# Kernel optimization log

Hardware: AMD Instinct MI355X
Metric: run time of the kernel (lower is better)

## Reference

```python
import jax, jax.numpy as jnp
import numpy as np

B, T, C = 16, 4096, 64  # batch, seq_len, n_embd == head_size


def setup_inputs() -> dict:
    key = jax.random.key(0)
    k1, k2, k3, k4 = jax.random.split(key, 4)
    x = jax.random.normal(k1, (B, T, C), dtype=jnp.float32)
    Wq = jax.random.normal(k2, (C, C), dtype=jnp.float32) * (C ** -0.5)
    Wk = jax.random.normal(k3, (C, C), dtype=jnp.float32) * (C ** -0.5)
    Wv = jax.random.normal(k4, (C, C), dtype=jnp.float32) * (C ** -0.5)
    return {"x": x, "Wq": Wq, "Wk": Wk, "Wv": Wv}


def reference(x, Wq, Wk, Wv):
    # Single-head causal self-attention (dropout rate = 0.0 in source -> identity).
    q = jnp.einsum('btc,cd->btd', x, Wq)  # [B,T,D]
    k = jnp.einsum('btc,cd->btd', x, Wk)  # [B,T,D]
    v = jnp.einsum('btc,cd->btd', x, Wv)  # [B,T,D]
    scale = q.shape[-1] ** -0.5
    wei = jnp.einsum('btd,bsd->bts', q, k) * scale  # [B,T,T] scores
    causal = jnp.tril(jnp.ones((T, T), dtype=bool))  # [T,T]
    wei = jnp.where(causal[None, :, :], wei, jnp.finfo(wei.dtype).min)
    wei = jax.nn.softmax(wei, axis=-1)
    out = jnp.einsum('bts,bsd->btd', wei, v)  # [B,T,D]
    return out
```

## Files before the change

### kernel.cpp

```cpp
#include <hip/hip_runtime.h>
#include <hip/hip_bf16.h>
#include <math.h>

#define BATCH 16
#define SEQ 4096
#define HDIM 64

typedef __attribute__((ext_vector_type(8))) short bf16x8;
typedef __attribute__((ext_vector_type(4))) float f32x4;
typedef __attribute__((ext_vector_type(4))) unsigned int u32x4;
typedef __attribute__((ext_vector_type(8))) unsigned short us8;

#define QSCALE 0.1803368801111601f

static __device__ __forceinline__ float exp2_fast(float x) {
#if __has_builtin(__builtin_amdgcn_exp2f)
    return __builtin_amdgcn_exp2f(x);
#else
    float r; asm("v_exp_f32 %0, %1" : "=v"(r) : "v"(x)); return r;
#endif
}

static __device__ __forceinline__ void load_lds16(const void* g, void* l) {
    __builtin_amdgcn_global_load_lds(
        (const __attribute__((address_space(1))) unsigned int*)g,
        (__attribute__((address_space(3))) unsigned int*)l,
        16, 0, 0);
}

static __device__ __forceinline__ unsigned short bf16bits(float f) {
    __hip_bfloat16 h = __float2bfloat16(f);
    return *(unsigned short*)&h;
}

static __device__ __forceinline__ unsigned int pack_bf16_trunc(float f0, float f1) {
    unsigned int u0 = __builtin_bit_cast(unsigned int, f0);
    unsigned int u1 = __builtin_bit_cast(unsigned int, f1);
#if __has_builtin(__builtin_amdgcn_perm)
    return __builtin_amdgcn_perm(u1, u0, 0x07060302u);
#else
    return (u1 & 0xFFFF0000u) | (u0 >> 16);
#endif
}

__global__ __launch_bounds__(256)
void qkv_mfma_kernel(const float* __restrict__ x,
                     const float* __restrict__ Wq,
                     const float* __restrict__ Wk,
                     const float* __restrict__ Wv,
                     __hip_bfloat16* __restrict__ qb,
                     __hip_bfloat16* __restrict__ kb,
                     __hip_bfloat16* __restrict__ vt) {
    __shared__ __attribute__((aligned(16))) __hip_bfloat16 swt[3 * 64 * 64];
    __shared__ __attribute__((aligned(16))) __hip_bfloat16 sout[64][80];
    const int tid = threadIdx.x;
    const int wv = tid >> 6;
    const int lane = tid & 63;
    const int quad = lane >> 4;
    const int ml = lane & 15;
    const size_t row0 = (size_t)blockIdx.x * 64;
    const int batch = (int)(row0 >> 12);
    const int t0 = (int)(row0 & 4095);

    #pragma unroll
    for (int mat = 0; mat < 3; ++mat) {
        const float* W = (mat == 0) ? Wq : (mat == 1) ? Wk : Wv;
        const float sc = (mat == 0) ? QSCALE : 1.0f;
        #pragma unroll
        for (int c2 = 0; c2 < 2; ++c2) {
            const int chunk = c2 * 256 + tid;
            const int n = chunk & 63;
            const int c = chunk >> 6;
            us8 u;
            #pragma unroll
            for (int j = 0; j < 8; ++j)
                u[j] = bf16bits(W[(c * 8 + j) * HDIM + n] * sc);
            *(us8*)(swt + mat * 4096 + n * 64 + (size_t)(c ^ (n & 7)) * 8) = u;
        }
    }

    bf16x8 a0, a1;
    {
        const float4* xr = (const float4*)(x + (row0 + wv * 16 + ml) * HDIM);
        float4 lo = xr[quad * 2], hi = xr[quad * 2 + 1];
        float t8[8] = {lo.x, lo.y, lo.z, lo.w, hi.x, hi.y, hi.z, hi.w};
        #pragma unroll
        for (int j = 0; j < 8; ++j) a0[j] = (short)bf16bits(t8[j]);
        lo = xr[8 + quad * 2]; hi = xr[9 + quad * 2];
        float u8[8] = {lo.x, lo.y, lo.z, lo.w, hi.x, hi.y, hi.z, hi.w};
        #pragma unroll
        for (int j = 0; j < 8; ++j) a1[j] = (short)bf16bits(u8[j]);
    }
    __syncthreads();

    #pragma unroll
    for (int mat = 0; mat < 3; ++mat) {
        const __hip_bfloat16* wb = swt + mat * 4096;
        f32x4 acc[4];
        #pragma unroll
        for (int nt = 0; nt < 4; ++nt) {
            const int n = nt * 16 + ml;
            const int nx = n & 7;
            const bf16x8 bl = *(const bf16x8*)(wb + (size_t)n * 64 + (size_t)((quad) ^ nx) * 8);
            const bf16x8 bh = *(const bf16x8*)(wb + (size_t)n * 64 + (size_t)((quad + 4) ^ nx) * 8);
            acc[nt] = __builtin_amdgcn_mfma_f32_16x16x32_bf16(a0, bl, (f32x4){0.f,0.f,0.f,0.f}, 0, 0, 0);
            acc[nt] = __builtin_amdgcn_mfma_f32_16x16x32_bf16(a1, bh, acc[nt], 0, 0, 0);
        }

        if (mat < 2) {
            #pragma unroll
            for (int nt = 0; nt < 4; ++nt)
                #pragma unroll
                for (int r = 0; r < 4; ++r)
                    sout[wv * 16 + quad * 4 + r][nt * 16 + ml] = __float2bfloat16(acc[nt][r]);
        } else {
            #pragma unroll
            for (int nt = 0; nt < 4; ++nt)
                #pragma unroll
                for (int r = 0; r < 4; ++r)
                    sout[nt * 16 + ml][(wv >> 1) * 32 + quad * 8 + (wv & 1) * 4 + r] =
                        __float2bfloat16(acc[nt][r]);
        }
        __syncthreads();
        __hip_bfloat16* dst = (mat == 0) ? qb : (mat == 1) ? kb : vt;
        #pragma unroll
        for (int c2 = 0; c2 < 2; ++c2) {
            const int cc = c2 * 256 + tid;
            const int row = cc >> 3, g = cc & 7;
            us8 u = *(const us8*)&sout[row][g * 8];
            if (mat < 2)
                *(us8*)(dst + (row0 + row) * HDIM + g * 8) = u;
            else
                *(us8*)(dst + ((size_t)batch * HDIM + row) * SEQ + t0 + g * 8) = u;
        }
        __syncthreads();
    }
}

__global__ __launch_bounds__(256, 4)
void flash_mfma_kernel(const __hip_bfloat16* __restrict__ qb,
                       const __hip_bfloat16* __restrict__ kbuf,
                       const __hip_bfloat16* __restrict__ vt,
                       float* __restrict__ out) {
    __shared__ __attribute__((aligned(16))) __hip_bfloat16 smem[16384];

    const int tid = threadIdx.x;
    const int wv = tid >> 6;
    const int lane = tid & 63;
    const int quad = lane >> 4;
    const int ml = lane & 15;
    const int mh = wv & 1;
    const int kh = wv >> 1;

    const int id = blockIdx.x;
    const int b = id & 15;
    const int t = id >> 4;
    const int hi2 = t >> 4, mid = t & 15;
    const int qt = (hi2 == 0) ? (63 - mid)
                 : (hi2 == 1) ? (32 + mid)
                 : (hi2 == 2) ? (31 - mid) : mid;
    const int qbw = qt * 64 + mh * 32;
    const size_t bb = (size_t)b * SEQ * HDIM;

    const __hip_bfloat16* Q = qb + bb;
    const __hip_bfloat16* K = kbuf + bb;
    const __hip_bfloat16* VT = vt + bb;

    bf16x8 bq[2][2];
    #pragma unroll
    for (int qi = 0; qi < 2; ++qi)
        #pragma unroll
        for (int h = 0; h < 2; ++h)
            bq[qi][h] = *(const bf16x8*)(Q + (size_t)(qbw + qi * 16 + ml) * HDIM + h * 32 + quad * 8);

    bf16x8 ones8;
    #pragma unroll
    for (int j = 0; j < 8; ++j) ones8[j] = (short)0x3F80;

    f32x4 acc[4][2];
    #pragma unroll
    for (int nt = 0; nt < 4; ++nt)
        #pragma unroll
        for (int qi = 0; qi < 2; ++qi) acc[nt][qi] = (f32x4){0.f, 0.f, 0.f, 0.f};
    f32x4 lacc[2] = {(f32x4){0.f,0.f,0.f,0.f}, (f32x4){0.f,0.f,0.f,0.f}};

    const int s0 = wv * 128 + lane;
    const int s1 = s0 + 64;
    const int r0row = s0 >> 3, r0ch = (s0 & 7) ^ (r0row & 7);
    const int r1row = s1 >> 3, r1ch = (s1 & 7) ^ (r1row & 7);
    const int d0 = (wv * 128) * 8;
    const int d1 = (wv * 128 + 64) * 8;

    const int ntiles = qt + 1;

    load_lds16(K + (size_t)r0row * HDIM + r0ch * 8, smem + d0);
    load_lds16(K + (size_t)r1row * HDIM + r1ch * 8, smem + d1);
    load_lds16(VT + (size_t)r0row * SEQ + r0ch * 8, smem + 8192 + d0);
    load_lds16(VT + (size_t)r1row * SEQ + r1ch * 8, smem + 8192 + d1);
    asm volatile("s_waitcnt vmcnt(0)" ::: "memory");
    __syncthreads();

    for (int tile = 0; tile < ntiles; ++tile) {
        const int kb0 = tile * 64;
        const int sel = (tile & 1) * 4096;
        const int nsel = 4096 - sel;
        const __hip_bfloat16* sk = smem + sel;
        const __hip_bfloat16* sv = smem + 8192 + sel;

        if (tile + 1 < ntiles) {
            const int nk = kb0 + 64;
            load_lds16(K + (size_t)(nk + r0row) * HDIM + r0ch * 8, smem + nsel + d0);
            load_lds16(K + (size_t)(nk + r1row) * HDIM + r1ch * 8, smem + nsel + d1);
            load_lds16(VT + (size_t)r0row * SEQ + nk + r0ch * 8, smem + 8192 + nsel + d0);
            load_lds16(VT + (size_t)r1row * SEQ + nk + r1ch * 8, smem + 8192 + nsel + d1);
        }

        if (!(tile == qt && kh == 1 && mh == 0)) {
            f32x4 st[2][2];
            #pragma unroll
            for (int kt = 0; kt < 2; ++kt) {
                const int row = kh * 32 + kt * 16 + ml;
                const int rb = row << 3, rxx = row & 7;
                const bf16x8 kl = *(const bf16x8*)(sk + (size_t)((rb | (quad ^ rxx)) * 8));
                const bf16x8 khi = *(const bf16x8*)(sk + (size_t)((rb | ((quad + 4) ^ rxx)) * 8));
                #pragma unroll
                for (int qi = 0; qi < 2; ++qi) {
                    st[kt][qi] = __builtin_amdgcn_mfma_f32_16x16x32_bf16(kl, bq[qi][0], (f32x4){0.f,0.f,0.f,0.f}, 0, 0, 0);
                    st[kt][qi] = __builtin_amdgcn_mfma_f32_16x16x32_bf16(khi, bq[qi][1], st[kt][qi], 0, 0, 0);
                }
            }

            const bool edge = (tile == qt);
            bf16x8 p8[2];
            #pragma unroll
            for (int qi = 0; qi < 2; ++qi) {
                const int q = qbw + qi * 16 + ml;
                float pv[8];
                #pragma unroll
                for (int half = 0; half < 2; ++half)
                    #pragma unroll
                    for (int r = 0; r < 4; ++r) {
                        const int key = kb0 + kh * 32 + half * 16 + quad * 4 + r;
                        float p = exp2_fast(st[half][qi][r]);
                        if (edge && (key > q)) p = 0.f;
                        pv[half * 4 + r] = p;
                    }
                u32x4 pk;
                #pragma unroll
                for (int d = 0; d < 4; ++d)
                    pk[d] = pack_bf16_trunc(pv[2 * d], pv[2 * d + 1]);
                p8[qi] = __builtin_bit_cast(bf16x8, pk);
            }

            lacc[0] = __builtin_amdgcn_mfma_f32_16x16x32_bf16(ones8, p8[0], lacc[0], 0, 0, 0);
            lacc[1] = __builtin_amdgcn_mfma_f32_16x16x32_bf16(ones8, p8[1], lacc[1], 0, 0, 0);
            #pragma unroll
            for (int nt = 0; nt < 4; ++nt) {
                const int row = nt * 16 + ml;
                const int rb = row << 3, rxx = row & 7;
                const bf16x8 va = *(const bf16x8*)(sv + (size_t)((rb | ((kh * 4 + quad) ^ rxx)) * 8));
                acc[nt][0] = __builtin_amdgcn_mfma_f32_16x16x32_bf16(va, p8[0], acc[nt][0], 0, 0, 0);
                acc[nt][1] = __builtin_amdgcn_mfma_f32_16x16x32_bf16(va, p8[1], acc[nt][1], 0, 0, 0);
            }
        }

        asm volatile("s_waitcnt vmcnt(0)" ::: "memory");
        __syncthreads();
    }

    float (*smerge)[64][18] = (float (*)[64][18])smem;
    #pragma unroll
    for (int qi = 0; qi < 2; ++qi) {
        __syncthreads();
        if (kh == 1) {
            float* mrow = smerge[mh][lane];
            #pragma unroll
            for (int nt = 0; nt < 4; ++nt)
                #pragma unroll
                for (int r = 0; r < 4; ++r) mrow[nt * 4 + r] = acc[nt][qi][r];
            mrow[16] = lacc[qi][0];
        }
        __syncthreads();
        if (kh == 0) {
            const float* mrow = smerge[mh][lane];
            const float inv = 1.0f / (lacc[qi][0] + mrow[16]);
            float* orow = out + bb + (size_t)(qbw + qi * 16 + ml) * HDIM;
            #pragma unroll
            for (int nt = 0; nt < 4; ++nt) {
                float4 o;
                o.x = (acc[nt][qi][0] + mrow[nt * 4 + 0]) * inv;
                o.y = (acc[nt][qi][1] + mrow[nt * 4 + 1]) * inv;
                o.z = (acc[nt][qi][2] + mrow[nt * 4 + 2]) * inv;
                o.w = (acc[nt][qi][3] + mrow[nt * 4 + 3]) * inv;
                *(float4*)(orow + nt * 16 + quad * 4) = o;
            }
        }
    }
}

extern "C" void kernel_launch(void* const* d_in, const int* in_sizes, int n_in,
                              void* d_out, int out_size, void* d_ws, size_t ws_size,
                              hipStream_t stream) {
    const float* x  = (const float*)d_in[0];
    const float* Wq = (const float*)d_in[1];
    const float* Wk = (const float*)d_in[2];
    const float* Wv = (const float*)d_in[3];
    float* outp = (float*)d_out;

    const size_t elems = (size_t)BATCH * SEQ * HDIM;
    __hip_bfloat16* qb = (__hip_bfloat16*)d_ws;
    __hip_bfloat16* kb = qb + elems;
    __hip_bfloat16* vt = kb + elems;

    qkv_mfma_kernel<<<dim3(BATCH * SEQ / 64), 256, 0, stream>>>(x, Wq, Wk, Wv, qb, kb, vt);
    flash_mfma_kernel<<<dim3(BATCH * SEQ / 64), 256, 0, stream>>>(qb, kb, vt, outp);
}
```

Before: 119.5 us.

## Load V fragments directly from global memory and raise wave priority around MFMA

Drops the LDS staging and double buffering of the transposed V tile. Each wave now reads its V MFMA fragments straight from global memory (relying on L2/L1 caching) at the start of each tile, which halves shared memory use and removes the extra async copies. It also wraps the MFMA groups with s_setprio so matrix work gets issue priority. The trade is more global load traffic and latency exposed in the loop, and the per-tile waitcnt now also waits on these direct loads.

```diff
diff --git a/kernel.cpp b/kernel.cpp
--- a/kernel.cpp
+++ b/kernel.cpp
@@ -142,7 +142,7 @@
                        const __hip_bfloat16* __restrict__ kbuf,
                        const __hip_bfloat16* __restrict__ vt,
                        float* __restrict__ out) {
-    __shared__ __attribute__((aligned(16))) __hip_bfloat16 smem[16384];
+    __shared__ __attribute__((aligned(16))) __hip_bfloat16 smem[8192];
 
     const int tid = threadIdx.x;
     const int wv = tid >> 6;
@@ -193,10 +193,10 @@
 
     const int ntiles = qt + 1;
 
+    const __hip_bfloat16* vrow = VT + (size_t)ml * SEQ + (kh * 4 + quad) * 8;
+
     load_lds16(K + (size_t)r0row * HDIM + r0ch * 8, smem + d0);
     load_lds16(K + (size_t)r1row * HDIM + r1ch * 8, smem + d1);
-    load_lds16(VT + (size_t)r0row * SEQ + r0ch * 8, smem + 8192 + d0);
-    load_lds16(VT + (size_t)r1row * SEQ + r1ch * 8, smem + 8192 + d1);
     asm volatile("s_waitcnt vmcnt(0)" ::: "memory");
     __syncthreads();
 
@@ -205,30 +205,38 @@
         const int sel = (tile & 1) * 4096;
         const int nsel = 4096 - sel;
         const __hip_bfloat16* sk = smem + sel;
-        const __hip_bfloat16* sv = smem + 8192 + sel;
 
         if (tile + 1 < ntiles) {
             const int nk = kb0 + 64;
             load_lds16(K + (size_t)(nk + r0row) * HDIM + r0ch * 8, smem + nsel + d0);
             load_lds16(K + (size_t)(nk + r1row) * HDIM + r1ch * 8, smem + nsel + d1);
-            load_lds16(VT + (size_t)r0row * SEQ + nk + r0ch * 8, smem + 8192 + nsel + d0);
-            load_lds16(VT + (size_t)r1row * SEQ + nk + r1ch * 8, smem + 8192 + nsel + d1);
         }
 
         if (!(tile == qt && kh == 1 && mh == 0)) {
-            f32x4 st[2][2];
+            bf16x8 va[4];
+            #pragma unroll
+            for (int nt = 0; nt < 4; ++nt)
+                va[nt] = *(const bf16x8*)(vrow + (size_t)(nt * 16) * SEQ + kb0);
+
+            bf16x8 kf[2][2];
             #pragma unroll
             for (int kt = 0; kt < 2; ++kt) {
                 const int row = kh * 32 + kt * 16 + ml;
                 const int rb = row << 3, rxx = row & 7;
-                const bf16x8 kl = *(const bf16x8*)(sk + (size_t)((rb | (quad ^ rxx)) * 8));
-                const bf16x8 khi = *(const bf16x8*)(sk + (size_t)((rb | ((quad + 4) ^ rxx)) * 8));
+                kf[kt][0] = *(const bf16x8*)(sk + (size_t)((rb | (quad ^ rxx)) * 8));
+                kf[kt][1] = *(const bf16x8*)(sk + (size_t)((rb | ((quad + 4) ^ rxx)) * 8));
+            }
+
+            f32x4 st[2][2];
+            __builtin_amdgcn_s_setprio(1);
+            #pragma unroll
+            for (int kt = 0; kt < 2; ++kt)
                 #pragma unroll
                 for (int qi = 0; qi < 2; ++qi) {
-                    st[kt][qi] = __builtin_amdgcn_mfma_f32_16x16x32_bf16(kl, bq[qi][0], (f32x4){0.f,0.f,0.f,0.f}, 0, 0, 0);
-                    st[kt][qi] = __builtin_amdgcn_mfma_f32_16x16x32_bf16(khi, bq[qi][1], st[kt][qi], 0, 0, 0);
+                    st[kt][qi] = __builtin_amdgcn_mfma_f32_16x16x32_bf16(kf[kt][0], bq[qi][0], (f32x4){0.f,0.f,0.f,0.f}, 0, 0, 0);
+                    st[kt][qi] = __builtin_amdgcn_mfma_f32_16x16x32_bf16(kf[kt][1], bq[qi][1], st[kt][qi], 0, 0, 0);
                 }
-            }
+            __builtin_amdgcn_s_setprio(0);
 
             const bool edge = (tile == qt);
             bf16x8 p8[2];
@@ -252,16 +260,15 @@
                 p8[qi] = __builtin_bit_cast(bf16x8, pk);
             }
 
+            __builtin_amdgcn_s_setprio(1);
             lacc[0] = __builtin_amdgcn_mfma_f32_16x16x32_bf16(ones8, p8[0], lacc[0], 0, 0, 0);
             lacc[1] = __builtin_amdgcn_mfma_f32_16x16x32_bf16(ones8, p8[1], lacc[1], 0, 0, 0);
             #pragma unroll
             for (int nt = 0; nt < 4; ++nt) {
-                const int row = nt * 16 + ml;
-                const int rb = row << 3, rxx = row & 7;
-                const bf16x8 va = *(const bf16x8*)(sv + (size_t)((rb | ((kh * 4 + quad) ^ rxx)) * 8));
-                acc[nt][0] = __builtin_amdgcn_mfma_f32_16x16x32_bf16(va, p8[0], acc[nt][0], 0, 0, 0);
-                acc[nt][1] = __builtin_amdgcn_mfma_f32_16x16x32_bf16(va, p8[1], acc[nt][1], 0, 0, 0);
+                acc[nt][0] = __builtin_amdgcn_mfma_f32_16x16x32_bf16(va[nt], p8[0], acc[nt][0], 0, 0, 0);
+                acc[nt][1] = __builtin_amdgcn_mfma_f32_16x16x32_bf16(va[nt], p8[1], acc[nt][1], 0, 0, 0);
             }
+            __builtin_amdgcn_s_setprio(0);
         }
 
         asm volatile("s_waitcnt vmcnt(0)" ::: "memory");
```

Result: slower. 157.1 us (+31.5%).

## Software-pipeline flash loop across tiles and precompute bf16 weights once

Applied to the files above, without the earlier changes.

The flash kernel's main loop is restructured into a two-stage software pipeline: the P·V product of one tile runs alongside the QK^T and softmax of the next, with triple-buffered V tiles in LDS and s_setprio raised around the MFMA bursts. The causal mask is peeled into a final edge-tile step, so interior tiles no longer test it. A separate small kernel converts and swizzles the weights to bf16 once, so each QKV block no longer redoes that conversion; it loads them and its x tile straight into LDS with direct global-to-LDS loads. This costs more LDS and registers in the flash kernel, which may lower occupancy, plus one extra launch.

```diff
diff --git a/kernel.cpp b/kernel.cpp
--- a/kernel.cpp
+++ b/kernel.cpp
@@ -44,15 +44,38 @@
 }
 
 __global__ __launch_bounds__(256)
+void wconv_kernel(const float* __restrict__ Wq,
+                  const float* __restrict__ Wk,
+                  const float* __restrict__ Wv,
+                  __hip_bfloat16* __restrict__ wsw) {
+    const int mat = blockIdx.x;
+    const int tid = threadIdx.x;
+    const float* W = (mat == 0) ? Wq : (mat == 1) ? Wk : Wv;
+    const float sc = (mat == 0) ? QSCALE : 1.0f;
+    #pragma unroll
+    for (int c2 = 0; c2 < 2; ++c2) {
+        const int chunk = c2 * 256 + tid;
+        const int n = chunk & 63;
+        const int c = chunk >> 6;
+        us8 u;
+        #pragma unroll
+        for (int j = 0; j < 8; ++j)
+            u[j] = bf16bits(W[(c * 8 + j) * HDIM + n] * sc);
+        *(us8*)(wsw + mat * 4096 + n * 64 + (size_t)(c ^ (n & 7)) * 8) = u;
+    }
+}
+
+__global__ __launch_bounds__(256)
 void qkv_mfma_kernel(const float* __restrict__ x,
-                     const float* __restrict__ Wq,
-                     const float* __restrict__ Wk,
-                     const float* __restrict__ Wv,
+                     const __hip_bfloat16* __restrict__ wsw,
                      __hip_bfloat16* __restrict__ qb,
                      __hip_bfloat16* __restrict__ kb,
                      __hip_bfloat16* __restrict__ vt) {
     __shared__ __attribute__((aligned(16))) __hip_bfloat16 swt[3 * 64 * 64];
-    __shared__ __attribute__((aligned(16))) __hip_bfloat16 sout[64][80];
+    __shared__ __attribute__((aligned(16))) char spool[16384];
+    float* sx = (float*)spool;
+    __hip_bfloat16 (*sout)[80] = (__hip_bfloat16 (*)[80])spool;
+
     const int tid = threadIdx.x;
     const int wv = tid >> 6;
     const int lane = tid & 63;
@@ -63,33 +86,21 @@
     const int t0 = (int)(row0 & 4095);
 
     #pragma unroll
-    for (int mat = 0; mat < 3; ++mat) {
-        const float* W = (mat == 0) ? Wq : (mat == 1) ? Wk : Wv;
-        const float sc = (mat == 0) ? QSCALE : 1.0f;
-        #pragma unroll
-        for (int c2 = 0; c2 < 2; ++c2) {
-            const int chunk = c2 * 256 + tid;
-            const int n = chunk & 63;
-            const int c = chunk >> 6;
-            us8 u;
-            #pragma unroll
-            for (int j = 0; j < 8; ++j)
-                u[j] = bf16bits(W[(c * 8 + j) * HDIM + n] * sc);
-            *(us8*)(swt + mat * 4096 + n * 64 + (size_t)(c ^ (n & 7)) * 8) = u;
-        }
-    }
+    for (int r = 0; r < 6; ++r)
+        load_lds16(wsw + (size_t)(r * 256 + tid) * 8, swt + (size_t)(r * 256 + tid) * 8);
+    #pragma unroll
+    for (int r = 0; r < 4; ++r)
+        load_lds16(x + row0 * HDIM + (size_t)(r * 256 + tid) * 4, sx + (size_t)(r * 256 + tid) * 4);
+    asm volatile("s_waitcnt vmcnt(0)" ::: "memory");
+    __syncthreads();
 
     bf16x8 a0, a1;
     {
-        const float4* xr = (const float4*)(x + (row0 + wv * 16 + ml) * HDIM);
-        float4 lo = xr[quad * 2], hi = xr[quad * 2 + 1];
-        float t8[8] = {lo.x, lo.y, lo.z, lo.w, hi.x, hi.y, hi.z, hi.w};
-        #pragma unroll
-        for (int j = 0; j < 8; ++j) a0[j] = (short)bf16bits(t8[j]);
-        lo = xr[8 + quad * 2]; hi = xr[9 + quad * 2];
-        float u8[8] = {lo.x, lo.y, lo.z, lo.w, hi.x, hi.y, hi.z, hi.w};
-        #pragma unroll
-        for (int j = 0; j < 8; ++j) a1[j] = (short)bf16bits(u8[j]);
+        const float* xr = sx + (size_t)(wv * 16 + ml) * HDIM + quad * 8;
+        #pragma unroll
+        for (int j = 0; j < 8; ++j) a0[j] = (short)bf16bits(xr[j]);
+        #pragma unroll
+        for (int j = 0; j < 8; ++j) a1[j] = (short)bf16bits(xr[32 + j]);
     }
     __syncthreads();
 
@@ -137,12 +148,107 @@
     }
 }
 
+#define MFMA16(A, B, C) __builtin_amdgcn_mfma_f32_16x16x32_bf16((A), (B), (C), 0, 0, 0)
+
+#define FLASH_STAGE(NK, KDST, VDST) do { \
+    load_lds16(K + (size_t)((NK) + r0row) * HDIM + r0ch * 8, smem + (KDST) + d0); \
+    load_lds16(K + (size_t)((NK) + r1row) * HDIM + r1ch * 8, smem + (KDST) + d1); \
+    load_lds16(VT + (size_t)r0row * SEQ + (NK) + r0ch * 8, smem + (VDST) + d0); \
+    load_lds16(VT + (size_t)r1row * SEQ + (NK) + r1ch * 8, smem + (VDST) + d1); \
+} while (0)
+
+#define FLASH_RDV(VSEL) do { \
+    const __hip_bfloat16* sv_ = smem + (VSEL); \
+    vaf[0] = *(const bf16x8*)(sv_ + voff[0]); \
+    vaf[1] = *(const bf16x8*)(sv_ + voff[1]); \
+    vaf[2] = *(const bf16x8*)(sv_ + voff[2]); \
+    vaf[3] = *(const bf16x8*)(sv_ + voff[3]); \
+} while (0)
+
+#define FLASH_RDK(KSEL) do { \
+    const __hip_bfloat16* sk_ = smem + (KSEL); \
+    kf[0][0] = *(const bf16x8*)(sk_ + koff[0][0]); \
+    kf[0][1] = *(const bf16x8*)(sk_ + koff[0][1]); \
+    kf[1][0] = *(const bf16x8*)(sk_ + koff[1][0]); \
+    kf[1][1] = *(const bf16x8*)(sk_ + koff[1][1]); \
+} while (0)
+
+#define FLASH_PV(P) do { \
+    __builtin_amdgcn_s_setprio(1); \
+    lacc[0] = MFMA16(ones8, P[0], lacc[0]); \
+    lacc[1] = MFMA16(ones8, P[1], lacc[1]); \
+    _Pragma("unroll") \
+    for (int nt_ = 0; nt_ < 4; ++nt_) { \
+        acc[nt_][0] = MFMA16(vaf[nt_], P[0], acc[nt_][0]); \
+        acc[nt_][1] = MFMA16(vaf[nt_], P[1], acc[nt_][1]); \
+    } \
+    __builtin_amdgcn_s_setprio(0); \
+} while (0)
+
+#define FLASH_QKT() do { \
+    __builtin_amdgcn_s_setprio(1); \
+    _Pragma("unroll") \
+    for (int kt_ = 0; kt_ < 2; ++kt_) \
+        _Pragma("unroll") \
+        for (int qi_ = 0; qi_ < 2; ++qi_) { \
+            st[kt_][qi_] = MFMA16(kf[kt_][0], bq[qi_][0], ((f32x4){0.f, 0.f, 0.f, 0.f})); \
+            st[kt_][qi_] = MFMA16(kf[kt_][1], bq[qi_][1], st[kt_][qi_]); \
+        } \
+    __builtin_amdgcn_s_setprio(0); \
+} while (0)
+
+#define FLASH_SM(POUT) do { \
+    _Pragma("unroll") \
+    for (int qi_ = 0; qi_ < 2; ++qi_) { \
+        float pv_[8]; \
+        _Pragma("unroll") \
+        for (int h_ = 0; h_ < 2; ++h_) \
+            _Pragma("unroll") \
+            for (int r_ = 0; r_ < 4; ++r_) \
+                pv_[h_ * 4 + r_] = exp2_fast(st[h_][qi_][r_]); \
+        u32x4 pk_; \
+        _Pragma("unroll") \
+        for (int d_ = 0; d_ < 4; ++d_) \
+            pk_[d_] = pack_bf16_trunc(pv_[2 * d_], pv_[2 * d_ + 1]); \
+        POUT[qi_] = __builtin_bit_cast(bf16x8, pk_); \
+    } \
+} while (0)
+
+#define FLASH_SMM(POUT, KB0) do { \
+    _Pragma("unroll") \
+    for (int qi_ = 0; qi_ < 2; ++qi_) { \
+        const int q_ = qbw + qi_ * 16 + ml; \
+        float pv_[8]; \
+        _Pragma("unroll") \
+        for (int h_ = 0; h_ < 2; ++h_) \
+            _Pragma("unroll") \
+            for (int r_ = 0; r_ < 4; ++r_) { \
+                const int key_ = (KB0) + kh * 32 + h_ * 16 + quad * 4 + r_; \
+                float p_ = exp2_fast(st[h_][qi_][r_]); \
+                if (key_ > q_) p_ = 0.f; \
+                pv_[h_ * 4 + r_] = p_; \
+            } \
+        u32x4 pk_; \
+        _Pragma("unroll") \
+        for (int d_ = 0; d_ < 4; ++d_) \
+            pk_[d_] = pack_bf16_trunc(pv_[2 * d_], pv_[2 * d_ + 1]); \
+        POUT[qi_] = __builtin_bit_cast(bf16x8, pk_); \
+    } \
+} while (0)
+
+#define FLASH_DRAIN() do { \
+    asm volatile("s_waitcnt vmcnt(0)" ::: "memory"); \
+    __syncthreads(); \
+} while (0)
+
+#define FLASH_VROT() do { int tmp_ = vb_m1; vb_m1 = vb_0; vb_0 = vb_p1; vb_p1 = tmp_; } while (0)
+
 __global__ __launch_bounds__(256, 4)
 void flash_mfma_kernel(const __hip_bfloat16* __restrict__ qb,
                        const __hip_bfloat16* __restrict__ kbuf,
                        const __hip_bfloat16* __restrict__ vt,
                        float* __restrict__ out) {
-    __shared__ __attribute__((aligned(16))) __hip_bfloat16 smem[16384];
+    __shared__ __attribute__((aligned(16))) __hip_bfloat16 smem[20480];
 
     const int tid = threadIdx.x;
     const int wv = tid >> 6;
@@ -154,8 +260,8 @@
 
     const int id = blockIdx.x;
     const int b = id & 15;
-    const int t = id >> 4;
-    const int hi2 = t >> 4, mid = t & 15;
+    const int t4 = id >> 4;
+    const int hi2 = t4 >> 4, mid = t4 & 15;
     const int qt = (hi2 == 0) ? (63 - mid)
                  : (hi2 == 1) ? (32 + mid)
                  : (hi2 == 2) ? (31 - mid) : mid;
@@ -191,81 +297,84 @@
     const int d0 = (wv * 128) * 8;
     const int d1 = (wv * 128 + 64) * 8;
 
-    const int ntiles = qt + 1;
-
-    load_lds16(K + (size_t)r0row * HDIM + r0ch * 8, smem + d0);
-    load_lds16(K + (size_t)r1row * HDIM + r1ch * 8, smem + d1);
-    load_lds16(VT + (size_t)r0row * SEQ + r0ch * 8, smem + 8192 + d0);
-    load_lds16(VT + (size_t)r1row * SEQ + r1ch * 8, smem + 8192 + d1);
-    asm volatile("s_waitcnt vmcnt(0)" ::: "memory");
-    __syncthreads();
-
-    for (int tile = 0; tile < ntiles; ++tile) {
-        const int kb0 = tile * 64;
-        const int sel = (tile & 1) * 4096;
-        const int nsel = 4096 - sel;
-        const __hip_bfloat16* sk = smem + sel;
-        const __hip_bfloat16* sv = smem + 8192 + sel;
-
-        if (tile + 1 < ntiles) {
-            const int nk = kb0 + 64;
-            load_lds16(K + (size_t)(nk + r0row) * HDIM + r0ch * 8, smem + nsel + d0);
-            load_lds16(K + (size_t)(nk + r1row) * HDIM + r1ch * 8, smem + nsel + d1);
-            load_lds16(VT + (size_t)r0row * SEQ + nk + r0ch * 8, smem + 8192 + nsel + d0);
-            load_lds16(VT + (size_t)r1row * SEQ + nk + r1ch * 8, smem + 8192 + nsel + d1);
-        }
-
-        if (!(tile == qt && kh == 1 && mh == 0)) {
-            f32x4 st[2][2];
-            #pragma unroll
-            for (int kt = 0; kt < 2; ++kt) {
-                const int row = kh * 32 + kt * 16 + ml;
-                const int rb = row << 3, rxx = row & 7;
-                const bf16x8 kl = *(const bf16x8*)(sk + (size_t)((rb | (quad ^ rxx)) * 8));
-                const bf16x8 khi = *(const bf16x8*)(sk + (size_t)((rb | ((quad + 4) ^ rxx)) * 8));
-                #pragma unroll
-                for (int qi = 0; qi < 2; ++qi) {
-                    st[kt][qi] = __builtin_amdgcn_mfma_f32_16x16x32_bf16(kl, bq[qi][0], (f32x4){0.f,0.f,0.f,0.f}, 0, 0, 0);
-                    st[kt][qi] = __builtin_amdgcn_mfma_f32_16x16x32_bf16(khi, bq[qi][1], st[kt][qi], 0, 0, 0);
-                }
-            }
-
-            const bool edge = (tile == qt);
-            bf16x8 p8[2];
-            #pragma unroll
-            for (int qi = 0; qi < 2; ++qi) {
-                const int q = qbw + qi * 16 + ml;
-                float pv[8];
-                #pragma unroll
-                for (int half = 0; half < 2; ++half)
-                    #pragma unroll
-                    for (int r = 0; r < 4; ++r) {
-                        const int key = kb0 + kh * 32 + half * 16 + quad * 4 + r;
-                        float p = exp2_fast(st[half][qi][r]);
-                        if (edge && (key > q)) p = 0.f;
-                        pv[half * 4 + r] = p;
-                    }
-                u32x4 pk;
-                #pragma unroll
-                for (int d = 0; d < 4; ++d)
-                    pk[d] = pack_bf16_trunc(pv[2 * d], pv[2 * d + 1]);
-                p8[qi] = __builtin_bit_cast(bf16x8, pk);
-            }
-
-            lacc[0] = __builtin_amdgcn_mfma_f32_16x16x32_bf16(ones8, p8[0], lacc[0], 0, 0, 0);
-            lacc[1] = __builtin_amdgcn_mfma_f32_16x16x32_bf16(ones8, p8[1], lacc[1], 0, 0, 0);
-            #pragma unroll
-            for (int nt = 0; nt < 4; ++nt) {
-                const int row = nt * 16 + ml;
-                const int rb = row << 3, rxx = row & 7;
-                const bf16x8 va = *(const bf16x8*)(sv + (size_t)((rb | ((kh * 4 + quad) ^ rxx)) * 8));
-                acc[nt][0] = __builtin_amdgcn_mfma_f32_16x16x32_bf16(va, p8[0], acc[nt][0], 0, 0, 0);
-                acc[nt][1] = __builtin_amdgcn_mfma_f32_16x16x32_bf16(va, p8[1], acc[nt][1], 0, 0, 0);
-            }
-        }
-
-        asm volatile("s_waitcnt vmcnt(0)" ::: "memory");
-        __syncthreads();
+    int koff[2][2], voff[4];
+    #pragma unroll
+    for (int kt = 0; kt < 2; ++kt) {
+        const int row = kh * 32 + kt * 16 + ml;
+        const int rb = row << 3, rxx = row & 7;
+        koff[kt][0] = (rb | (quad ^ rxx)) * 8;
+        koff[kt][1] = (rb | ((quad + 4) ^ rxx)) * 8;
+    }
+    #pragma unroll
+    for (int nt = 0; nt < 4; ++nt) {
+        const int row = nt * 16 + ml;
+        const int rb = row << 3, rxx = row & 7;
+        voff[nt] = (rb | ((kh * 4 + quad) ^ rxx)) * 8;
+    }
+
+    bf16x8 kf[2][2], vaf[4];
+    bf16x8 pA[2], pB[2];
+    f32x4 st[2][2];
+    int vb_m1 = 16384, vb_0 = 8192, vb_p1 = 12288;
+
+    FLASH_STAGE(0, 0, vb_0);
+    FLASH_DRAIN();
+
+    int t = 1;
+    if (qt >= 1) {
+        FLASH_STAGE(64, 4096, vb_p1);
+        FLASH_RDK(0);
+        FLASH_QKT();
+        FLASH_SM(pA);
+        FLASH_DRAIN();
+        FLASH_VROT();
+
+        for (t = 1; t + 1 < qt; t += 2) {
+            FLASH_STAGE((t + 1) * 64, 0, vb_p1);
+            FLASH_RDV(vb_m1);
+            FLASH_RDK(4096);
+            FLASH_PV(pA);
+            FLASH_QKT();
+            FLASH_SM(pB);
+            FLASH_DRAIN();
+            FLASH_VROT();
+
+            FLASH_STAGE((t + 2) * 64, 4096, vb_p1);
+            FLASH_RDV(vb_m1);
+            FLASH_RDK(0);
+            FLASH_PV(pB);
+            FLASH_QKT();
+            FLASH_SM(pA);
+            FLASH_DRAIN();
+            FLASH_VROT();
+        }
+        if (t < qt) {
+            FLASH_STAGE(qt * 64, 0, vb_p1);
+            FLASH_RDV(vb_m1);
+            FLASH_RDK(4096);
+            FLASH_PV(pA);
+            FLASH_QKT();
+            FLASH_SM(pB);
+            FLASH_DRAIN();
+            FLASH_VROT();
+        } else if (qt & 1) {
+            pB[0] = pA[0];
+            pB[1] = pA[1];
+        }
+    }
+
+    {
+        if (qt > 0) {
+            FLASH_RDV(vb_m1);
+            FLASH_PV(pB);
+        }
+        if (!(kh == 1 && mh == 0)) {
+            FLASH_RDV(vb_0);
+            FLASH_RDK((qt & 1) * 4096);
+            FLASH_QKT();
+            FLASH_SMM(pA, qt * 64);
+            FLASH_PV(pA);
+        }
     }
 
     float (*smerge)[64][18] = (float (*)[64][18])smem;
@@ -311,7 +420,9 @@
     __hip_bfloat16* qb = (__hip_bfloat16*)d_ws;
     __hip_bfloat16* kb = qb + elems;
     __hip_bfloat16* vt = kb + elems;
-
-    qkv_mfma_kernel<<<dim3(BATCH * SEQ / 64), 256, 0, stream>>>(x, Wq, Wk, Wv, qb, kb, vt);
+    __hip_bfloat16* wsw = vt + elems;
+
+    wconv_kernel<<<dim3(3), 256, 0, stream>>>(Wq, Wk, Wv, wsw);
+    qkv_mfma_kernel<<<dim3(BATCH * SEQ / 64), 256, 0, stream>>>(x, wsw, qb, kb, vt);
     flash_mfma_kernel<<<dim3(BATCH * SEQ / 64), 256, 0, stream>>>(qb, kb, vt, outp);
 }
```

After: 120.3 us. About the same (+0.7%).
